# Performance work log

Hardware: AMD Instinct MI355X
Metric: run time of the kernel (lower is better)

Reference implementation:

```python
import jax, jax.numpy as jnp
import numpy as np

EPS = 1e-5

def conv1x1(x, W, b):
    # x: (B,C,H,W), W: (O,C), b: (O,)
    return jnp.einsum('bchw,oc->bohw', x, W) + b[None, :, None, None]

def setup_inputs() -> dict:
    key = jax.random.key(0)
    ks = jax.random.split(key, 16)
    B, C_in, C1, D, K, H, Wd = 8, 512, 256, 128, 32, 96, 96
    s = lambda k, shape, fan: jax.random.normal(k, shape, jnp.float32) * (1.0 / np.sqrt(fan))
    return {
        'X': jax.random.normal(ks[0], (B, C_in, H, Wd), jnp.float32),
        'W_theta': s(ks[1], (C1, C_in), C_in), 'b_theta': jnp.zeros((C1,), jnp.float32),
        'W_phi': s(ks[2], (C1, C_in), C_in), 'b_phi': jnp.zeros((C1,), jnp.float32),
        'W_g': s(ks[3], (C1, C_in), C_in), 'b_g': jnp.zeros((C1,), jnp.float32),
        'W2': s(ks[4], (C_in, C1), C1), 'b2': jnp.zeros((C_in,), jnp.float32),
        'W3': s(ks[5], (D, C_in), C_in), 'b3': jnp.zeros((D,), jnp.float32),
        'codewords': jax.random.normal(ks[6], (K, D), jnp.float32),
        'scale': -jax.random.uniform(ks[7], (K,), jnp.float32),  # Deep-TEN init: U(-1,0)
        'W_fc': s(ks[8], (C_in, D), D), 'b_fc': jnp.zeros((C_in,), jnp.float32),
    }

def reference(X, W_theta, b_theta, W_phi, b_phi, W_g, b_g, W2, b2, W3, b3,
              codewords, scale, W_fc, b_fc):
    B, C_in, H, Wd = X.shape
    C1 = W_theta.shape[0]
    D, K = W3.shape[0], codewords.shape[0]
    N = H * Wd
    # --- non-local (channel-attention) block ---
    theta = conv1x1(X, W_theta, b_theta).reshape(B, C1, N)          # (B,C1,N)
    phi = conv1x1(X, W_phi, b_phi).reshape(B, C1, N)                # (B,C1,N)
    g = conv1x1(X, W_g, b_g).reshape(B, C1, N)                      # (B,C1,N)
    f = jax.nn.softmax(jnp.einsum('bcn,bdn->bcd', theta, phi), axis=-1)  # (B,C1,C1)
    y = jnp.einsum('bcd,bdn->bcn', f, g).reshape(B, C1, H, Wd)
    z = conv1x1(y, W2, b2) + X                                      # (B,C_in,H,W)
    # --- Deep-TEN encoding ---
    z_ = conv1x1(z, W3, b3)                                         # (B,D,H,W)
    x = z_.reshape(B, D, N).transpose(0, 2, 1)                      # (B,N,D)
    # squared L2 distances to codewords without (B,N,K,D) residuals
    dist = (jnp.sum(x * x, -1, keepdims=True)
            - 2.0 * jnp.einsum('bnd,kd->bnk', x, codewords)
            + jnp.sum(codewords * codewords, -1))                   # (B,N,K)
    A = jax.nn.softmax(scale * dist, axis=-1)                       # (B,N,K)
    # E_k = sum_i A_ik (x_i - c_k)
    E = jnp.einsum('bnk,bnd->bkd', A, x) - A.sum(1)[..., None] * codewords  # (B,K,D)
    # --- training-mode batch norm over K channels (no affine) ---
    mean = E.mean(axis=(0, 2), keepdims=True)
    var = E.var(axis=(0, 2), keepdims=True)
    e = jax.nn.relu((E - mean) * jax.lax.rsqrt(var + EPS))
    Es = e.sum(axis=1)                                              # (B,D)
    gamma = jax.nn.sigmoid(Es @ W_fc.T + b_fc)                      # (B,C_in)
    return z * gamma[:, :, None, None]
```

## Files before the change

### kernel.cpp

```cpp
#include <hip/hip_runtime.h>


typedef unsigned short u16;

#define Bb 8
#define Cc 512
#define C1 256
#define Dd 128
#define Kk 32
#define Nn 9216

typedef __attribute__((ext_vector_type(8))) short short8v;
typedef __attribute__((ext_vector_type(4))) short short4v;
typedef __attribute__((ext_vector_type(4))) float f32x4;

__device__ __forceinline__ float b2f(u16 u) {
  union { unsigned int i; float f; } v; v.i = ((unsigned int)u) << 16; return v.f;
}
__device__ __forceinline__ u16 f2b(float f) {
  union { float f; unsigned int i; } v; v.f = f;
  unsigned int x = v.i;
  return (u16)((x + 0x7fffu + ((x >> 16) & 1u)) >> 16);
}

__device__ __forceinline__ float4 load4(const float* p) { return *(const float4*)p; }
__device__ __forceinline__ float4 load4(const u16* p) {
  ushort4 q = *(const ushort4*)p;
  return make_float4(b2f(q.x), b2f(q.y), b2f(q.z), b2f(q.w));
}
__device__ __forceinline__ void store4(float* p, float a, float b, float c, float d) {
  *(float4*)p = make_float4(a, b, c, d);
}

__device__ __forceinline__ float waveSum(float v) {
  #pragma unroll
  for (int o = 32; o > 0; o >>= 1) v += __shfl_xor(v, o);
  return v;
}
__device__ __forceinline__ float waveMax(float v) {
  #pragma unroll
  for (int o = 32; o > 0; o >>= 1) v = fmaxf(v, __shfl_xor(v, o));
  return v;
}
__device__ __forceinline__ float blockSum256(float v) {
  __shared__ float sm[4];
  v = waveSum(v);
  if ((threadIdx.x & 63) == 0) sm[threadIdx.x >> 6] = v;
  __syncthreads();
  float r = sm[0] + sm[1] + sm[2] + sm[3];
  __syncthreads();
  return r;
}
__device__ __forceinline__ float blockMax256(float v) {
  __shared__ float sm[4];
  v = waveMax(v);
  if ((threadIdx.x & 63) == 0) sm[threadIdx.x >> 6] = v;
  __syncthreads();
  float r = fmaxf(fmaxf(sm[0], sm[1]), fmaxf(sm[2], sm[3]));
  __syncthreads();
  return r;
}

__device__ __forceinline__ f32x4 mfma_bf16_16x16x32(short8v a, short8v b, f32x4 c) {
  asm("v_mfma_f32_16x16x32_bf16 %0, %1, %2, %0" : "+v"(c) : "v"(a), "v"(b));
  return c;
}

__device__ __forceinline__ int fsw(int r) { return (r ^ (r >> 2) ^ (r >> 4)) & 3; }

__device__ __forceinline__ void cvt2(float x0, float x1, unsigned int& h, unsigned int& l) {
  asm("v_cvt_pk_bf16_f32 %0, %1, %2" : "=v"(h) : "v"(x0), "v"(x1));
  union { unsigned int u; float f; } fa, fb;
  fa.u = h << 16; fb.u = h & 0xffff0000u;
  float r0 = x0 - fa.f, r1 = x1 - fb.f;
  asm("v_cvt_pk_bf16_f32 %0, %1, %2" : "=v"(l) : "v"(r0), "v"(r1));
}

__device__ __forceinline__ void storeC4(float* p, float4 v) { *(float4*)p = v; }
__device__ __forceinline__ void storeC4(u16* p, float4 v) {
  ushort4 q; q.x = f2b(v.x); q.y = f2b(v.y); q.z = f2b(v.z); q.w = f2b(v.w);
  *(ushort4*)p = q;
}

template<typename TO, int OMODE, bool ADDI>
__global__ __launch_bounds__(256, 3) void gemm_mfma(
    const float* __restrict__ A, const float* __restrict__ B, TO* __restrict__ C,
    int N, int K,
    long long sA, long long sB, long long sC,
    const float* __restrict__ biasRow, long long sBias,
    int gnx, int gny)
{
  __shared__ __align__(16) u16 Asm_[2][128][40];
  __shared__ __align__(16) u16 Bsm_[2][128][40];

  int id = blockIdx.x;
  {
    const int nwg = gridDim.x;
    if ((nwg & 7) == 0) id = (id & 7) * (nwg >> 3) + (id >> 3);
  }
  const int per = gnx * gny;
  const int b = id / per;
  const int rem = id - b * per;
  const int by = rem % gny;
  const int bx = rem / gny;
  A += b * sA; B += b * sB; C += b * sC;
  const int m0 = by * 128, n0 = bx * 128;

  const int t = threadIdx.x;
  const int w = t >> 6, lane = t & 63;
  const int wr = w >> 1, wc = w & 1;
  const int lr = lane & 15, lq = lane >> 4;

  const int sar = t >> 1, sak = (t & 1) * 16;
  const int kg2 = t >> 4, ng = t & 15;

  float ra[16];
  float rb[16];

  auto loadA = [&](int k0) {
    const float* p = A + (long long)(m0 + sar) * K + (k0 + sak);
    #pragma unroll
    for (int i = 0; i < 4; ++i) {
      float4 v = *(const float4*)(p + i * 4);
      ra[i*4+0] = v.x; ra[i*4+1] = v.y; ra[i*4+2] = v.z; ra[i*4+3] = v.w;
    }
  };
  auto loadB = [&](int k0) {
    const float* p = B + (long long)(k0 + kg2 * 2) * N + (n0 + ng * 8);
    #pragma unroll
    for (int i = 0; i < 2; ++i) {
      float4 v0 = *(const float4*)(p + (long long)i * N);
      float4 v1 = *(const float4*)(p + (long long)i * N + 4);
      rb[i*8+0]=v0.x; rb[i*8+1]=v0.y; rb[i*8+2]=v0.z; rb[i*8+3]=v0.w;
      rb[i*8+4]=v1.x; rb[i*8+5]=v1.y; rb[i*8+6]=v1.z; rb[i*8+7]=v1.w;
    }
  };

  auto stage = [&]() {
    {
      const int f = fsw(sar);
      #pragma unroll
      for (int h = 0; h < 2; ++h) {
        const int col = ((((sak >> 3) + h) ^ f) << 3);
        union { unsigned int u[4]; short8v v; } H, L;
        #pragma unroll
        for (int p = 0; p < 4; ++p) cvt2(ra[h*8+2*p], ra[h*8+2*p+1], H.u[p], L.u[p]);
        *(short8v*)&Asm_[0][sar][col] = H.v;
        *(short8v*)&Asm_[1][sar][col] = L.v;
      }
    }
    {
      const int blk = kg2 >> 2, sub = 2 * (kg2 & 3);
      #pragma unroll
      for (int j = 0; j < 8; ++j) {
        const int n = ng * 8 + j;
        const int col = ((blk ^ fsw(n)) << 3) + sub;
        unsigned int H, L;
        cvt2(rb[j], rb[8 + j], H, L);
        *(unsigned int*)&Bsm_[0][n][col] = H;
        *(unsigned int*)&Bsm_[1][n][col] = L;
      }
    }
  };

  f32x4 acc[4][4];
  #pragma unroll
  for (int im = 0; im < 4; ++im)
    #pragma unroll
    for (int in = 0; in < 4; ++in)
      acc[im][in] = f32x4{0.f, 0.f, 0.f, 0.f};

  loadA(0); loadB(0);
  for (int k0 = 0; k0 < K; k0 += 32) {
    stage();
    if (k0 + 32 < K) { loadA(k0 + 32); loadB(k0 + 32); }
    __syncthreads();
    short8v af[2][4];
    #pragma unroll
    for (int im = 0; im < 4; ++im) {
      const int r = wr * 64 + im * 16 + lr;
      const int col = ((lq ^ fsw(r)) << 3);
      af[0][im] = *(const short8v*)&Asm_[0][r][col];
      af[1][im] = *(const short8v*)&Asm_[1][r][col];
    }
    #pragma unroll
    for (int in = 0; in < 4; ++in) {
      const int rB = wc * 64 + in * 16 + lr;
      const int colB = ((lq ^ fsw(rB)) << 3);
      short8v bh = *(const short8v*)&Bsm_[0][rB][colB];
      short8v bl = *(const short8v*)&Bsm_[1][rB][colB];
      #pragma unroll
      for (int im = 0; im < 4; ++im) {
        acc[im][in] = mfma_bf16_16x16x32(af[0][im], bh, acc[im][in]);
        acc[im][in] = mfma_bf16_16x16x32(af[0][im], bl, acc[im][in]);
        acc[im][in] = mfma_bf16_16x16x32(af[1][im], bh, acc[im][in]);
      }
    }
    __syncthreads();
  }
  asm volatile("s_nop 7\n\ts_nop 7\n\ts_nop 7");

  if constexpr (OMODE == 1) {
    const float* bb = biasRow + (long long)b * sBias;
    #pragma unroll
    for (int im = 0; im < 4; ++im) {
      #pragma unroll
      for (int in = 0; in < 4; ++in) {
        const f32x4 a = acc[im][in];
        const int gc = n0 + wc * 64 + in * 16 + lr;
        const int d0b = wr * 64 + im * 16 + lq * 4;
        float4 v = make_float4(a[0] + bb[d0b + 0], a[1] + bb[d0b + 1],
                               a[2] + bb[d0b + 2], a[3] + bb[d0b + 3]);
        storeC4(&C[(long long)gc * Dd + d0b], v);
      }
    }
  } else {
    #pragma unroll
    for (int im = 0; im < 4; ++im) {
      #pragma unroll
      for (int in = 0; in < 4; ++in) {
        const f32x4 a = acc[im][in];
        const int gc = n0 + wc * 64 + in * 16 + lr;
        #pragma unroll
        for (int p = 0; p < 4; ++p) {
          const int gr = m0 + wr * 64 + im * 16 + lq * 4 + p;
          float v = a[p];
          if (biasRow) v += biasRow[b * sBias + gr];
          if (ADDI && gr == gc) v += 1.f;
          C[(long long)gr * N + gc] = v;
        }
      }
    }
  }
}

__device__ __constant__ int PIa[10] = {0,0,0,0,1,1,1,2,2,3};
__device__ __constant__ int PJa[10] = {0,1,2,3,1,2,3,2,3,3};

__global__ __launch_bounds__(256, 3) void gxxt_kernel(
    const float* __restrict__ X, float* __restrict__ part,
    int numKS, int kChunk)
{
  __shared__ __align__(16) u16 Asm_[2][128][40];
  __shared__ __align__(16) u16 Bsm_[2][64][40];

  int id = blockIdx.x;
  {
    const int nwg = gridDim.x;
    if ((nwg & 7) == 0) id = (id & 7) * (nwg >> 3) + (id >> 3);
  }
  const int sub = id % 20;
  const int pair = sub >> 1, jh = sub & 1;
  const int rest = id / 20;
  const int ks = rest % numKS;
  const int b = rest / numKS;
  const int i0 = PIa[pair] * 128, j0 = PJa[pair] * 128;
  const bool same = (i0 == j0);
  const float* Xb = X + (long long)b * Cc * Nn;
  const int kBeg = ks * kChunk, kEnd = kBeg + kChunk;

  const int t = threadIdx.x;
  const int w = t >> 6, lane = t & 63;
  const int wr = w >> 1, wc = w & 1;
  const int lr = lane & 15, lq = lane >> 4;
  const int sar = t >> 1, sak = (t & 1) * 16;
  const int sbr = t >> 2, sbk = (t & 3) * 8;

  float ra[16], rb[8];

  auto loadA = [&](int k0) {
    const float* p = Xb + (long long)(i0 + sar) * Nn + (k0 + sak);
    #pragma unroll
    for (int i = 0; i < 4; ++i) {
      float4 v = *(const float4*)(p + i * 4);
      ra[i*4+0] = v.x; ra[i*4+1] = v.y; ra[i*4+2] = v.z; ra[i*4+3] = v.w;
    }
  };
  auto loadB = [&](int k0) {
    const float* p = Xb + (long long)(j0 + jh * 64 + sbr) * Nn + (k0 + sbk);
    float4 v0 = *(const float4*)(p);
    float4 v1 = *(const float4*)(p + 4);
    rb[0]=v0.x; rb[1]=v0.y; rb[2]=v0.z; rb[3]=v0.w;
    rb[4]=v1.x; rb[5]=v1.y; rb[6]=v1.z; rb[7]=v1.w;
  };
  auto stageA = [&]() {
    const int f = fsw(sar);
    #pragma unroll
    for (int h = 0; h < 2; ++h) {
      const int col = ((((sak >> 3) + h) ^ f) << 3);
      union { unsigned int u[4]; short8v v; } Hv, Lv;
      #pragma unroll
      for (int p = 0; p < 4; ++p) cvt2(ra[h*8+2*p], ra[h*8+2*p+1], Hv.u[p], Lv.u[p]);
      *(short8v*)&Asm_[0][sar][col] = Hv.v;
      *(short8v*)&Asm_[1][sar][col] = Lv.v;
    }
  };
  auto stageB = [&]() {
    const int col = (((sbk >> 3) ^ fsw(sbr)) << 3);
    union { unsigned int u[4]; short8v v; } Hv, Lv;
    #pragma unroll
    for (int p = 0; p < 4; ++p) cvt2(rb[2*p], rb[2*p+1], Hv.u[p], Lv.u[p]);
    *(short8v*)&Bsm_[0][sbr][col] = Hv.v;
    *(short8v*)&Bsm_[1][sbr][col] = Lv.v;
  };

  f32x4 acc[4][2];
  #pragma unroll
  for (int im = 0; im < 4; ++im)
    #pragma unroll
    for (int in = 0; in < 2; ++in)
      acc[im][in] = f32x4{0.f, 0.f, 0.f, 0.f};

  loadA(kBeg);
  if (!same) loadB(kBeg);
  for (int k0 = kBeg; k0 < kEnd; k0 += 32) {
    stageA();
    if (!same) stageB();
    if (k0 + 32 < kEnd) { loadA(k0 + 32); if (!same) loadB(k0 + 32); }
    __syncthreads();
    short8v af[2][4];
    #pragma unroll
    for (int im = 0; im < 4; ++im) {
      const int r = wr * 64 + im * 16 + lr;
      const int col = ((lq ^ fsw(r)) << 3);
      af[0][im] = *(const short8v*)&Asm_[0][r][col];
      af[1][im] = *(const short8v*)&Asm_[1][r][col];
    }
    #pragma unroll
    for (int in = 0; in < 2; ++in) {
      const int rloc = wc * 32 + in * 16 + lr;
      short8v bh, bl;
      if (same) {
        const int r = jh * 64 + rloc;
        const int colB = ((lq ^ fsw(r)) << 3);
        bh = *(const short8v*)&Asm_[0][r][colB];
        bl = *(const short8v*)&Asm_[1][r][colB];
      } else {
        const int colB = ((lq ^ fsw(rloc)) << 3);
        bh = *(const short8v*)&Bsm_[0][rloc][colB];
        bl = *(const short8v*)&Bsm_[1][rloc][colB];
      }
      #pragma unroll
      for (int im = 0; im < 4; ++im) {
        acc[im][in] = mfma_bf16_16x16x32(af[0][im], bh, acc[im][in]);
        acc[im][in] = mfma_bf16_16x16x32(af[0][im], bl, acc[im][in]);
        acc[im][in] = mfma_bf16_16x16x32(af[1][im], bh, acc[im][in]);
      }
    }
    __syncthreads();
  }
  asm volatile("s_nop 7\n\ts_nop 7\n\ts_nop 7");

  float* Cp = part + ((long long)(ks * Bb + b) * 10 + pair) * 16384 + jh * 64;
  #pragma unroll
  for (int im = 0; im < 4; ++im) {
    #pragma unroll
    for (int in = 0; in < 2; ++in) {
      const f32x4 a = acc[im][in];
      const int gc = wc * 32 + in * 16 + lr;
      #pragma unroll
      for (int p = 0; p < 4; ++p) {
        const int gr = wr * 64 + im * 16 + lq * 4 + p;
        Cp[gr * 128 + gc] = a[p];
      }
    }
  }
}

__global__ __launch_bounds__(256) void gred_kernel(const float* __restrict__ part,
    float* __restrict__ G, int numKS) {
  __shared__ float sm[64][129];
  const int pair = blockIdx.x % 10, b = blockIdx.x / 10;
  const int i0 = PIa[pair] * 128, j0 = PJa[pair] * 128;
  float* Gb = G + (long long)b * Cc * Cc;
  const long long ksStr = (long long)Bb * 10 * 16384;
  const float* p0 = part + ((long long)b * 10 + pair) * 16384;
  const int t = threadIdx.x;
  for (int half = 0; half < 2; ++half) {
    const int r0 = half * 64;
    __syncthreads();
    for (int rep = 0; rep < 32; ++rep) {
      int idx = r0 * 128 + rep * 256 + t;
      float s = 0.f;
      for (int ks = 0; ks < numKS; ++ks) s += p0[(long long)ks * ksStr + idx];
      int r = (idx >> 7) - r0, c = idx & 127;
      sm[r][c] = s;
      Gb[(long long)(i0 + r0 + r) * Cc + (j0 + c)] = s;
    }
    if (i0 != j0) {
      __syncthreads();
      for (int rep = 0; rep < 32; ++rep) {
        int o = rep * 256 + t;
        int rr = o >> 6, cc = o & 63;
        Gb[(long long)(j0 + rr) * Cc + (i0 + r0 + cc)] = sm[cc][rr];
      }
    }
  }
}

template<bool TRANSB>
__global__ __launch_bounds__(256) void gemm64(
    const float* __restrict__ A, const float* __restrict__ B, float* __restrict__ C,
    int M, int N, int K,
    long long sA, long long sB, long long sC,
    const float* __restrict__ biasRow, long long sBias)
{
  const int bz = blockIdx.z;
  A += (long long)bz * sA;
  B += (long long)bz * sB;
  C += (long long)bz * sC;
  const int m0 = blockIdx.y * 64, n0 = blockIdx.x * 64;
  __shared__ __align__(16) float As[16][64];
  __shared__ __align__(16) float Bs[16][64];
  const int t = threadIdx.x;
  const int lr = t >> 2, lk = (t & 3) << 2;
  const int tm = (t >> 4) << 2, tn = (t & 15) << 2;
  float acc[4][4] = {};
  for (int k0 = 0; k0 < K; k0 += 16) {
    {
      float4 a = load4(A + (long long)(m0 + lr) * K + (k0 + lk));
      As[lk + 0][lr] = a.x; As[lk + 1][lr] = a.y; As[lk + 2][lr] = a.z; As[lk + 3][lr] = a.w;
    }
    if (TRANSB) {
      float4 b = load4(B + (long long)(n0 + lr) * K + (k0 + lk));
      Bs[lk + 0][lr] = b.x; Bs[lk + 1][lr] = b.y; Bs[lk + 2][lr] = b.z; Bs[lk + 3][lr] = b.w;
    } else {
      const int kr = t >> 4, nc = (t & 15) << 2;
      float4 b = load4(B + (long long)(k0 + kr) * N + (n0 + nc));
      *(float4*)&Bs[kr][nc] = b;
    }
    __syncthreads();
    #pragma unroll
    for (int kk = 0; kk < 16; ++kk) {
      const float4 av = *(const float4*)&As[kk][tm];
      const float4 bv = *(const float4*)&Bs[kk][tn];
      acc[0][0] = fmaf(av.x, bv.x, acc[0][0]);
      acc[0][1] = fmaf(av.x, bv.y, acc[0][1]);
      acc[0][2] = fmaf(av.x, bv.z, acc[0][2]);
      acc[0][3] = fmaf(av.x, bv.w, acc[0][3]);
      acc[1][0] = fmaf(av.y, bv.x, acc[1][0]);
      acc[1][1] = fmaf(av.y, bv.y, acc[1][1]);
      acc[1][2] = fmaf(av.y, bv.z, acc[1][2]);
      acc[1][3] = fmaf(av.y, bv.w, acc[1][3]);
      acc[2][0] = fmaf(av.z, bv.x, acc[2][0]);
      acc[2][1] = fmaf(av.z, bv.y, acc[2][1]);
      acc[2][2] = fmaf(av.z, bv.z, acc[2][2]);
      acc[2][3] = fmaf(av.z, bv.w, acc[2][3]);
      acc[3][0] = fmaf(av.w, bv.x, acc[3][0]);
      acc[3][1] = fmaf(av.w, bv.y, acc[3][1]);
      acc[3][2] = fmaf(av.w, bv.z, acc[3][2]);
      acc[3][3] = fmaf(av.w, bv.w, acc[3][3]);
    }
    __syncthreads();
  }
  #pragma unroll
  for (int i = 0; i < 4; ++i) {
    const int m = m0 + tm + i;
    float bias = biasRow ? biasRow[bz * sBias + m] : 0.f;
    store4(C + (long long)m * N + (n0 + tn),
           acc[i][0] + bias, acc[i][1] + bias, acc[i][2] + bias, acc[i][3] + bias);
  }
}

__global__ __launch_bounds__(256) void rowsum_kernel(const float* __restrict__ X,
                                                     float* __restrict__ s, int N) {
  long long row = blockIdx.x;
  const float* p = X + row * N;
  float acc = 0.f;
  for (int i = threadIdx.x * 4; i < N; i += 1024) {
    float4 v = *(const float4*)(p + i);
    acc += (v.x + v.y) + (v.z + v.w);
  }
  acc = blockSum256(acc);
  if (threadIdx.x == 0) s[row] = acc;
}

__global__ __launch_bounds__(256) void gemv2_kernel(const float* __restrict__ Wth,
    const float* __restrict__ Wph, const float* __restrict__ s,
    float* __restrict__ u, float* __restrict__ v) {
  int b = blockIdx.x & 7, sel = blockIdx.x >> 3;
  const float* W = sel ? Wph : Wth;
  float* out = sel ? v : u;
  __shared__ float ssm[Cc];
  for (int i = threadIdx.x; i < Cc; i += 256) ssm[i] = s[b * Cc + i];
  __syncthreads();
  int i = threadIdx.x;
  const float* wr = W + i * Cc;
  float acc = 0.f;
  for (int k = 0; k < Cc; ++k) acc = fmaf(wr[k], ssm[k], acc);
  out[b * C1 + i] = acc;
}

__global__ __launch_bounds__(256) void softmax_kernel(float* __restrict__ L,
    const float* __restrict__ bth, const float* __restrict__ bph,
    const float* __restrict__ u, const float* __restrict__ v,
    const float* __restrict__ bg, float* __restrict__ w) {
  __shared__ float bgs[C1];
  int row = blockIdx.x;
  int b = row >> 8, i = row & 255;
  int j = threadIdx.x;
  bgs[j] = bg[j];
  float bt = bth[i], bp = bph[j];
  long long idx = (long long)row * C1 + j;
  float val = L[idx] + bt * v[b * C1 + j] + u[b * C1 + i] * bp + (float)Nn * bt * bp;
  float mx = blockMax256(val);
  float p = expf(val - mx);
  float sm = blockSum256(p);
  float f = p / sm;
  L[idx] = f;
  float ws = blockSum256(f * bgs[j]);
  if (j == 0) w[row] = ws;
}

__global__ __launch_bounds__(256) void q_kernel(const float* __restrict__ W2,
                                                const float* __restrict__ b2v,
                                                const float* __restrict__ w,
                                                float* __restrict__ q) {
  int gi = blockIdx.x * 256 + threadIdx.x;
  int b = gi >> 9, c = gi & 511;
  __shared__ float wsm[C1];
  wsm[threadIdx.x] = w[b * C1 + threadIdx.x];
  __syncthreads();
  const float* wr = W2 + c * C1;
  float acc = b2v[c];
  for (int i = 0; i < C1; ++i) acc = fmaf(wr[i], wsm[i], acc);
  q[gi] = acc;
}

__global__ __launch_bounds__(256) void zqbias_kernel(const float* __restrict__ W3,
    const float* __restrict__ b3, const float* __restrict__ q, float* __restrict__ zqb) {
  int gi = blockIdx.x * 256 + threadIdx.x;
  int b = gi >> 7, d = gi & 127;
  const float* wr = W3 + d * Cc;
  const float* qr = q + b * Cc;
  float acc = b3[d];
  for (int c = 0; c < Cc; ++c) acc = fmaf(wr[c], qr[c], acc);
  zqb[gi] = acc;
}

template<typename ZT>
__global__ __launch_bounds__(256) void enc_kernel(
    const ZT* __restrict__ zq,
    const float* __restrict__ cw,
    const float* __restrict__ sc,
    float* __restrict__ Eraw8,
    float* __restrict__ Asum8)
{
  __shared__ float csm[Kk][Dd + 1];
  __shared__ float cc[Kk], ssm[Kk];
  __shared__ float sA[Kk][256 + 1];
  __shared__ float zs[16][Dd + 4];
  const int tid = threadIdx.x;
  const int b = blockIdx.y;
  const int slot = blockIdx.x & 7;
  const int n0 = blockIdx.x * 256;

  #pragma unroll
  for (int r = 0; r < 16; ++r) {
    int idx = r * 256 + tid;
    csm[idx >> 7][idx & 127] = cw[idx];
  }
  if (tid < Kk) ssm[tid] = sc[tid];
  __syncthreads();
  if (tid < Kk) {
    float a = 0.f;
    for (int d = 0; d < Dd; ++d) { float cv = csm[tid][d]; a = fmaf(cv, cv, a); }
    cc[tid] = a;
  }
  __syncthreads();

  const ZT* zrow = zq + ((long long)b * Nn + n0 + tid) * Dd;
  float dots[Kk];
  #pragma unroll
  for (int k = 0; k < Kk; ++k) dots[k] = 0.f;
  float xx = 0.f;
  for (int d = 0; d < Dd; d += 4) {
    float4 xv = load4(zrow + d);
    xx = fmaf(xv.x, xv.x, xx); xx = fmaf(xv.y, xv.y, xx);
    xx = fmaf(xv.z, xv.z, xx); xx = fmaf(xv.w, xv.w, xx);
    #pragma unroll
    for (int k = 0; k < Kk; ++k) {
      float dk = dots[k];
      dk = fmaf(csm[k][d + 0], xv.x, dk);
      dk = fmaf(csm[k][d + 1], xv.y, dk);
      dk = fmaf(csm[k][d + 2], xv.z, dk);
      dk = fmaf(csm[k][d + 3], xv.w, dk);
      dots[k] = dk;
    }
  }
  float mx = -1e30f;
  #pragma unroll
  for (int k = 0; k < Kk; ++k) {
    float l = ssm[k] * (xx - 2.f * dots[k] + cc[k]);
    dots[k] = l;
    mx = fmaxf(mx, l);
  }
  float sum = 0.f;
  #pragma unroll
  for (int k = 0; k < Kk; ++k) { float p = expf(dots[k] - mx); dots[k] = p; sum += p; }
  float inv = 1.f / sum;
  #pragma unroll
  for (int k = 0; k < Kk; ++k) sA[k][tid] = dots[k] * inv;
  __syncthreads();
  if (tid < Kk) {
    float s = 0.f;
    for (int p = 0; p < 256; ++p) s += sA[tid][p];
    atomicAdd(&Asum8[((long long)slot * Bb + b) * Kk + tid], s);
  }

  float acc[16];
  #pragma unroll
  for (int j = 0; j < 16; ++j) acc[j] = 0.f;
  const int k = tid & 31, d0 = (tid >> 5) * 16;
  const int spx = tid >> 4, sd = (tid & 15) * 8;
  for (int it = 0; it < 16; ++it) {
    __syncthreads();
    {
      const ZT* src = zq + ((long long)b * Nn + n0 + it * 16 + spx) * Dd + sd;
      float4 a4 = load4(src);
      float4 b4 = load4(src + 4);
      *(float4*)&zs[spx][sd] = a4;
      *(float4*)&zs[spx][sd + 4] = b4;
    }
    __syncthreads();
    #pragma unroll
    for (int p = 0; p < 16; ++p) {
      float a = sA[k][it * 16 + p];
      #pragma unroll
      for (int j = 0; j < 16; ++j) acc[j] = fmaf(a, zs[p][d0 + j], acc[j]);
    }
  }
  float* Ep = Eraw8 + (((long long)slot * Bb + b) * Kk + k) * Dd + d0;
  #pragma unroll
  for (int j = 0; j < 16; ++j) atomicAdd(Ep + j, acc[j]);
}

__global__ __launch_bounds__(256) void bn_kernel(const float* __restrict__ Eraw8,
    const float* __restrict__ Asum8, const float* __restrict__ cw, float* __restrict__ Es) {
  __shared__ float sas[8];
  int k = blockIdx.x, tid = threadIdx.x;
  if (tid < 8) {
    float a = 0.f;
    for (int sl = 0; sl < 8; ++sl) a += Asum8[((long long)sl * Bb + tid) * Kk + k];
    sas[tid] = a;
  }
  __syncthreads();
  float vals[4], s = 0.f, s2 = 0.f;
  #pragma unroll
  for (int r = 0; r < 4; ++r) {
    int i = r * 256 + tid;
    int b = i >> 7, d = i & 127;
    float e = 0.f;
    for (int sl = 0; sl < 8; ++sl)
      e += Eraw8[(((long long)sl * Bb + b) * Kk + k) * Dd + d];
    e -= sas[b] * cw[k * Dd + d];
    vals[r] = e; s += e; s2 = fmaf(e, e, s2);
  }
  s = blockSum256(s);
  s2 = blockSum256(s2);
  float mean = s * (1.f / 1024.f);
  float var = fmaxf(s2 * (1.f / 1024.f) - mean * mean, 0.f);
  float rs = rsqrtf(var + 1e-5f);
  #pragma unroll
  for (int r = 0; r < 4; ++r) {
    int i = r * 256 + tid;
    int b = i >> 7, d = i & 127;
    float e = (vals[r] - mean) * rs;
    if (e > 0.f) atomicAdd(&Es[b * Dd + d], e);
  }
}

__global__ __launch_bounds__(256) void gamma_kernel(const float* __restrict__ Es,
    const float* __restrict__ Wfc, const float* __restrict__ bfc,
    float* __restrict__ gam, float* __restrict__ q) {
  int gi = blockIdx.x * 256 + threadIdx.x;
  int b = gi >> 9, c = gi & 511;
  __shared__ float esm[Dd];
  if (threadIdx.x < Dd) esm[threadIdx.x] = Es[b * Dd + threadIdx.x];
  __syncthreads();
  const float* wr = Wfc + c * Dd;
  float acc = bfc[c];
  for (int d = 0; d < Dd; ++d) acc = fmaf(wr[d], esm[d], acc);
  float g = 1.f / (1.f + expf(-acc));
  gam[gi] = g;
  q[gi] *= g;
}

__global__ __launch_bounds__(256) void scaleP_kernel(float* __restrict__ P,
    const float* __restrict__ gam) {
  long long f = ((long long)blockIdx.x * 256 + threadIdx.x) * 4;
  int b = (int)(f >> 18), c = (int)((f >> 9) & 511);
  float g = gam[b * Cc + c];
  float4 v = *(const float4*)(P + f);
  store4(P + f, v.x * g, v.y * g, v.z * g, v.w * g);
}

extern "C" void kernel_launch(void* const* d_in, const int* in_sizes, int n_in,
                              void* d_out, int out_size, void* d_ws, size_t ws_size,
                              hipStream_t stream) {
  const float* X   = (const float*)d_in[0];
  const float* Wth = (const float*)d_in[1];
  const float* bth = (const float*)d_in[2];
  const float* Wph = (const float*)d_in[3];
  const float* bph = (const float*)d_in[4];
  const float* Wg  = (const float*)d_in[5];
  const float* bg  = (const float*)d_in[6];
  const float* W2  = (const float*)d_in[7];
  const float* b2v = (const float*)d_in[8];
  const float* W3  = (const float*)d_in[9];
  const float* b3v = (const float*)d_in[10];
  const float* CW  = (const float*)d_in[11];
  const float* SC  = (const float*)d_in[12];
  const float* Wfc = (const float*)d_in[13];
  const float* bfc = (const float*)d_in[14];
  float* out = (float*)d_out;
  float* wsf = (float*)d_ws;

  const long long szL   = (long long)Bb * C1 * C1;
  const long long szRA  = (long long)Bb * Cc * Cc;
  const long long szRB  = (long long)Bb * C1 * Cc;
  long long off = 0;
  float* s_   = wsf + off; off += Bb * Cc;
  float* u_   = wsf + off; off += Bb * C1;
  float* v_   = wsf + off; off += Bb * C1;
  float* w_   = wsf + off; off += Bb * C1;
  float* q_   = wsf + off; off += Bb * Cc;
  float* Eraw_= wsf + off; off += (long long)Bb * Kk * Dd;
  float* Es_  = wsf + off; off += Bb * Dd;
  float* Asum_= wsf + off; off += Bb * Kk;
  float* gam_ = wsf + off; off += Bb * Cc;
  float* L_   = wsf + off; off += szL;
  float* regA = wsf + off; off += szRA;
  float* regB = wsf + off; off += szRB;
  const long long baseFloats = off;
  float* tail = wsf + off;
  const long long ZQ_F  = (long long)Bb * Dd * Nn;
  const long long tailFloats = (long long)(ws_size / 4) - baseFloats;
  const bool big = tailFloats >= ZQ_F;
  const int numKS = big ? 6 : 2;
  float* part = tail;
  float* zqf  = tail;
  u16*   zqh  = (u16*)tail;
  float* R_   = L_;
  float* zqb_ = u_;
  float* E8_  = regB;
  float* A8_  = regB + 262144;
  (void)Eraw_; (void)Asum_;

  const long long strX = (long long)Cc * Nn;
  const long long sG = (long long)Cc * Cc;
  const long long sU = (long long)C1 * Cc;
  const long long sL = (long long)C1 * C1;
  const long long sR = (long long)Dd * Cc;

  rowsum_kernel<<<Bb * Cc, 256, 0, stream>>>(X, s_, Nn);
  gxxt_kernel<<<dim3(20 * numKS * Bb), 256, 0, stream>>>(X, part, numKS, Nn / numKS);
  gred_kernel<<<dim3(10 * Bb), 256, 0, stream>>>(part, regA, numKS);
  gemm_mfma<float, 0, false><<<dim3(64), 256, 0, stream>>>(
      Wth, regA, regB, Cc, Cc, 0, sG, sU, nullptr, 0, 4, 2);
  gemv2_kernel<<<16, 256, 0, stream>>>(Wth, Wph, s_, u_, v_);
  gemm64<true><<<dim3(4, 4, Bb), 256, 0, stream>>>(
      regB, Wph, L_, C1, C1, Cc, sU, 0, sL, nullptr, 0);
  softmax_kernel<<<Bb * C1, 256, 0, stream>>>(L_, bth, bph, u_, v_, bg, w_);
  gemm_mfma<float, 0, false><<<dim3(64), 256, 0, stream>>>(
      L_, Wg, regB, Cc, C1, sL, 0, sU, nullptr, 0, 4, 2);
  q_kernel<<<16, 256, 0, stream>>>(W2, b2v, w_, q_);
  gemm_mfma<float, 0, true><<<dim3(128), 256, 0, stream>>>(
      W2, regB, regA, Cc, C1, 0, sU, sG, nullptr, 0, 4, 4);
  hipMemsetAsync(regB, 0, (size_t)(262144 + 2048) * 4, stream);
  hipMemsetAsync(Es_, 0, (size_t)(Bb * Dd) * 4, stream);
  gemm_mfma<float, 0, false><<<dim3(32), 256, 0, stream>>>(
      W3, regA, R_, Cc, Cc, 0, sG, sR, nullptr, 0, 4, 1);
  zqbias_kernel<<<4, 256, 0, stream>>>(W3, b3v, q_, zqb_);
  if (big) {
    gemm_mfma<float, 1, false><<<dim3(576), 256, 0, stream>>>(
        R_, X, zqf, Nn, Cc, sR, strX, (long long)Dd * Nn, zqb_, Dd, 72, 1);
    enc_kernel<float><<<dim3(36, Bb), 256, 0, stream>>>(zqf, CW, SC, E8_, A8_);
  } else {
    gemm_mfma<u16, 1, false><<<dim3(576), 256, 0, stream>>>(
        R_, X, zqh, Nn, Cc, sR, strX, (long long)Dd * Nn, zqb_, Dd, 72, 1);
    enc_kernel<u16><<<dim3(36, Bb), 256, 0, stream>>>(zqh, CW, SC, E8_, A8_);
  }
  bn_kernel<<<Kk, 256, 0, stream>>>(E8_, A8_, CW, Es_);
  gamma_kernel<<<16, 256, 0, stream>>>(Es_, Wfc, bfc, gam_, q_);
  scaleP_kernel<<<2048, 256, 0, stream>>>(regA, gam_);
  gemm_mfma<float, 0, false><<<dim3(2304), 256, 0, stream>>>(
      regA, X, out, Nn, Cc, sG, strX, strX, q_, Cc, 72, 4);
  (void)in_sizes; (void)n_in; (void)out_size;
}
```

Baseline: 957.8 us.

## Fuse rowsum into Gram kernel, fold gamma scaling into final GEMM, pad B LDS

Result: no change. 947.5 us (-1.1%).

```diff
diff --git a/kernel.cpp b/kernel.cpp
--- a/kernel.cpp
+++ b/kernel.cpp
@@ -10,6 +10,8 @@
 #define Kk 32
 #define Nn 9216
 
+#define BIDX(n, c) (((n) * 40) + (((n) >> 3) * 8) + (c))
+
 typedef __attribute__((ext_vector_type(8))) short short8v;
 typedef __attribute__((ext_vector_type(4))) short short4v;
 typedef __attribute__((ext_vector_type(4))) float f32x4;
@@ -88,10 +90,11 @@
     int N, int K,
     long long sA, long long sB, long long sC,
     const float* __restrict__ biasRow, long long sBias,
+    const float* __restrict__ scaleA,
     int gnx, int gny)
 {
   __shared__ __align__(16) u16 Asm_[2][128][40];
-  __shared__ __align__(16) u16 Bsm_[2][128][40];
+  __shared__ __align__(16) u16 Bsm_[2][5248];
 
   int id = blockIdx.x;
   {
@@ -114,6 +117,8 @@
   const int sar = t >> 1, sak = (t & 1) * 16;
   const int kg2 = t >> 4, ng = t & 15;
 
+  const float gA = scaleA ? scaleA[b * sBias + m0 + sar] : 1.f;
+
   float ra[16];
   float rb[16];
 
@@ -144,7 +149,8 @@
         const int col = ((((sak >> 3) + h) ^ f) << 3);
         union { unsigned int u[4]; short8v v; } H, L;
         #pragma unroll
-        for (int p = 0; p < 4; ++p) cvt2(ra[h*8+2*p], ra[h*8+2*p+1], H.u[p], L.u[p]);
+        for (int p = 0; p < 4; ++p)
+          cvt2(ra[h*8+2*p] * gA, ra[h*8+2*p+1] * gA, H.u[p], L.u[p]);
         *(short8v*)&Asm_[0][sar][col] = H.v;
         *(short8v*)&Asm_[1][sar][col] = L.v;
       }
@@ -157,8 +163,8 @@
         const int col = ((blk ^ fsw(n)) << 3) + sub;
         unsigned int H, L;
         cvt2(rb[j], rb[8 + j], H, L);
-        *(unsigned int*)&Bsm_[0][n][col] = H;
-        *(unsigned int*)&Bsm_[1][n][col] = L;
+        *(unsigned int*)&Bsm_[0][BIDX(n, col)] = H;
+        *(unsigned int*)&Bsm_[1][BIDX(n, col)] = L;
       }
     }
   };
@@ -187,8 +193,8 @@
     for (int in = 0; in < 4; ++in) {
       const int rB = wc * 64 + in * 16 + lr;
       const int colB = ((lq ^ fsw(rB)) << 3);
-      short8v bh = *(const short8v*)&Bsm_[0][rB][colB];
-      short8v bl = *(const short8v*)&Bsm_[1][rB][colB];
+      short8v bh = *(const short8v*)&Bsm_[0][BIDX(rB, colB)];
+      short8v bl = *(const short8v*)&Bsm_[1][BIDX(rB, colB)];
       #pragma unroll
       for (int im = 0; im < 4; ++im) {
         acc[im][in] = mfma_bf16_16x16x32(af[0][im], bh, acc[im][in]);
@@ -239,10 +245,10 @@
 
 __global__ __launch_bounds__(256, 3) void gxxt_kernel(
     const float* __restrict__ X, float* __restrict__ part,
-    int numKS, int kChunk)
+    int numKS, int kChunk, float* __restrict__ sOut)
 {
   __shared__ __align__(16) u16 Asm_[2][128][40];
-  __shared__ __align__(16) u16 Bsm_[2][64][40];
+  __shared__ __align__(16) u16 Bsm_[2][2624];
 
   int id = blockIdx.x;
   {
@@ -256,6 +262,7 @@
   const int b = rest / numKS;
   const int i0 = PIa[pair] * 128, j0 = PJa[pair] * 128;
   const bool same = (i0 == j0);
+  const bool doSum = same && (jh == 0);
   const float* Xb = X + (long long)b * Cc * Nn;
   const int kBeg = ks * kChunk, kEnd = kBeg + kChunk;
 
@@ -267,6 +274,7 @@
   const int sbr = t >> 2, sbk = (t & 3) * 8;
 
   float ra[16], rb[8];
+  float rs = 0.f;
 
   auto loadA = [&](int k0) {
     const float* p = Xb + (long long)(i0 + sar) * Nn + (k0 + sak);
@@ -300,8 +308,8 @@
     union { unsigned int u[4]; short8v v; } Hv, Lv;
     #pragma unroll
     for (int p = 0; p < 4; ++p) cvt2(rb[2*p], rb[2*p+1], Hv.u[p], Lv.u[p]);
-    *(short8v*)&Bsm_[0][sbr][col] = Hv.v;
-    *(short8v*)&Bsm_[1][sbr][col] = Lv.v;
+    *(short8v*)&Bsm_[0][BIDX(sbr, col)] = Hv.v;
+    *(short8v*)&Bsm_[1][BIDX(sbr, col)] = Lv.v;
   };
 
   f32x4 acc[4][2];
@@ -314,6 +322,10 @@
   loadA(kBeg);
   if (!same) loadB(kBeg);
   for (int k0 = kBeg; k0 < kEnd; k0 += 32) {
+    if (doSum) {
+      #pragma unroll
+      for (int j = 0; j < 16; ++j) rs += ra[j];
+    }
     stageA();
     if (!same) stageB();
     if (k0 + 32 < kEnd) { loadA(k0 + 32); if (!same) loadB(k0 + 32); }
@@ -337,8 +349,8 @@
         bl = *(const short8v*)&Asm_[1][r][colB];
       } else {
         const int colB = ((lq ^ fsw(rloc)) << 3);
-        bh = *(const short8v*)&Bsm_[0][rloc][colB];
-        bl = *(const short8v*)&Bsm_[1][rloc][colB];
+        bh = *(const short8v*)&Bsm_[0][BIDX(rloc, colB)];
+        bl = *(const short8v*)&Bsm_[1][BIDX(rloc, colB)];
       }
       #pragma unroll
       for (int im = 0; im < 4; ++im) {
@@ -350,6 +362,8 @@
     __syncthreads();
   }
   asm volatile("s_nop 7\n\ts_nop 7\n\ts_nop 7");
+
+  if (doSum) atomicAdd(&sOut[b * Cc + i0 + sar], rs);
 
   float* Cp = part + ((long long)(ks * Bb + b) * 10 + pair) * 16384 + jh * 64;
   #pragma unroll
@@ -462,19 +476,6 @@
   }
 }
 
-__global__ __launch_bounds__(256) void rowsum_kernel(const float* __restrict__ X,
-                                                     float* __restrict__ s, int N) {
-  long long row = blockIdx.x;
-  const float* p = X + row * N;
-  float acc = 0.f;
-  for (int i = threadIdx.x * 4; i < N; i += 1024) {
-    float4 v = *(const float4*)(p + i);
-    acc += (v.x + v.y) + (v.z + v.w);
-  }
-  acc = blockSum256(acc);
-  if (threadIdx.x == 0) s[row] = acc;
-}
-
 __global__ __launch_bounds__(256) void gemv2_kernel(const float* __restrict__ Wth,
     const float* __restrict__ Wph, const float* __restrict__ s,
     float* __restrict__ u, float* __restrict__ v) {
@@ -684,15 +685,6 @@
   float g = 1.f / (1.f + expf(-acc));
   gam[gi] = g;
   q[gi] *= g;
-}
-
-__global__ __launch_bounds__(256) void scaleP_kernel(float* __restrict__ P,
-    const float* __restrict__ gam) {
-  long long f = ((long long)blockIdx.x * 256 + threadIdx.x) * 4;
-  int b = (int)(f >> 18), c = (int)((f >> 9) & 511);
-  float g = gam[b * Cc + c];
-  float4 v = *(const float4*)(P + f);
-  store4(P + f, v.x * g, v.y * g, v.z * g, v.w * g);
 }
 
 extern "C" void kernel_launch(void* const* d_in, const int* in_sizes, int n_in,
@@ -726,7 +718,7 @@
   float* w_   = wsf + off; off += Bb * C1;
   float* q_   = wsf + off; off += Bb * Cc;
   float* Eraw_= wsf + off; off += (long long)Bb * Kk * Dd;
-  float* Es_  = wsf + off; off += Bb * Dd;
+  float* EsL_ = wsf + off; off += Bb * Dd;
   float* Asum_= wsf + off; off += Bb * Kk;
   float* gam_ = wsf + off; off += Bb * Cc;
   float* L_   = wsf + off; off += szL;
@@ -737,7 +729,7 @@
   const long long ZQ_F  = (long long)Bb * Dd * Nn;
   const long long tailFloats = (long long)(ws_size / 4) - baseFloats;
   const bool big = tailFloats >= ZQ_F;
-  const int numKS = big ? 6 : 2;
+  const int numKS = big ? 4 : 2;
   float* part = tail;
   float* zqf  = tail;
   u16*   zqh  = (u16*)tail;
@@ -745,7 +737,8 @@
   float* zqb_ = u_;
   float* E8_  = regB;
   float* A8_  = regB + 262144;
-  (void)Eraw_; (void)Asum_;
+  float* Es_  = regB + 264192;
+  (void)Eraw_; (void)Asum_; (void)EsL_;
 
   const long long strX = (long long)Cc * Nn;
   const long long sG = (long long)Cc * Cc;
@@ -753,38 +746,36 @@
   const long long sL = (long long)C1 * C1;
   const long long sR = (long long)Dd * Cc;
 
-  rowsum_kernel<<<Bb * Cc, 256, 0, stream>>>(X, s_, Nn);
-  gxxt_kernel<<<dim3(20 * numKS * Bb), 256, 0, stream>>>(X, part, numKS, Nn / numKS);
+  hipMemsetAsync(s_, 0, (size_t)(Bb * Cc) * 4, stream);
+  gxxt_kernel<<<dim3(20 * numKS * Bb), 256, 0, stream>>>(X, part, numKS, Nn / numKS, s_);
   gred_kernel<<<dim3(10 * Bb), 256, 0, stream>>>(part, regA, numKS);
   gemm_mfma<float, 0, false><<<dim3(64), 256, 0, stream>>>(
-      Wth, regA, regB, Cc, Cc, 0, sG, sU, nullptr, 0, 4, 2);
+      Wth, regA, regB, Cc, Cc, 0, sG, sU, nullptr, 0, nullptr, 4, 2);
   gemv2_kernel<<<16, 256, 0, stream>>>(Wth, Wph, s_, u_, v_);
   gemm64<true><<<dim3(4, 4, Bb), 256, 0, stream>>>(
       regB, Wph, L_, C1, C1, Cc, sU, 0, sL, nullptr, 0);
   softmax_kernel<<<Bb * C1, 256, 0, stream>>>(L_, bth, bph, u_, v_, bg, w_);
   gemm_mfma<float, 0, false><<<dim3(64), 256, 0, stream>>>(
-      L_, Wg, regB, Cc, C1, sL, 0, sU, nullptr, 0, 4, 2);
+      L_, Wg, regB, Cc, C1, sL, 0, sU, nullptr, 0, nullptr, 4, 2);
   q_kernel<<<16, 256, 0, stream>>>(W2, b2v, w_, q_);
   gemm_mfma<float, 0, true><<<dim3(128), 256, 0, stream>>>(
-      W2, regB, regA, Cc, C1, 0, sU, sG, nullptr, 0, 4, 4);
-  hipMemsetAsync(regB, 0, (size_t)(262144 + 2048) * 4, stream);
-  hipMemsetAsync(Es_, 0, (size_t)(Bb * Dd) * 4, stream);
+      W2, regB, regA, Cc, C1, 0, sU, sG, nullptr, 0, nullptr, 4, 4);
+  hipMemsetAsync(regB, 0, (size_t)(262144 + 2048 + 1024) * 4, stream);
   gemm_mfma<float, 0, false><<<dim3(32), 256, 0, stream>>>(
-      W3, regA, R_, Cc, Cc, 0, sG, sR, nullptr, 0, 4, 1);
+      W3, regA, R_, Cc, Cc, 0, sG, sR, nullptr, 0, nullptr, 4, 1);
   zqbias_kernel<<<4, 256, 0, stream>>>(W3, b3v, q_, zqb_);
   if (big) {
     gemm_mfma<float, 1, false><<<dim3(576), 256, 0, stream>>>(
-        R_, X, zqf, Nn, Cc, sR, strX, (long long)Dd * Nn, zqb_, Dd, 72, 1);
+        R_, X, zqf, Nn, Cc, sR, strX, (long long)Dd * Nn, zqb_, Dd, nullptr, 72, 1);
     enc_kernel<float><<<dim3(36, Bb), 256, 0, stream>>>(zqf, CW, SC, E8_, A8_);
   } else {
     gemm_mfma<u16, 1, false><<<dim3(576), 256, 0, stream>>>(
-        R_, X, zqh, Nn, Cc, sR, strX, (long long)Dd * Nn, zqb_, Dd, 72, 1);
+        R_, X, zqh, Nn, Cc, sR, strX, (long long)Dd * Nn, zqb_, Dd, nullptr, 72, 1);
     enc_kernel<u16><<<dim3(36, Bb), 256, 0, stream>>>(zqh, CW, SC, E8_, A8_);
   }
   bn_kernel<<<Kk, 256, 0, stream>>>(E8_, A8_, CW, Es_);
   gamma_kernel<<<16, 256, 0, stream>>>(Es_, Wfc, bfc, gam_, q_);
-  scaleP_kernel<<<2048, 256, 0, stream>>>(regA, gam_);
   gemm_mfma<float, 0, false><<<dim3(2304), 256, 0, stream>>>(
-      regA, X, out, Nn, Cc, sG, strX, strX, q_, Cc, 72, 4);
+      regA, X, out, Nn, Cc, sG, strX, strX, q_, Cc, gam_, 72, 4);
   (void)in_sizes; (void)n_in; (void)out_size;
 }
```

## Fuse X row sums into Gram kernel and merge memsets

Applied to the files above, without the earlier changes.

New measurement: 895.9 us. 6.5% less time.

```diff
diff --git a/kernel.cpp b/kernel.cpp
--- a/kernel.cpp
+++ b/kernel.cpp
@@ -239,7 +239,7 @@
 
 __global__ __launch_bounds__(256, 3) void gxxt_kernel(
     const float* __restrict__ X, float* __restrict__ part,
-    int numKS, int kChunk)
+    int numKS, int kChunk, float* __restrict__ sP)
 {
   __shared__ __align__(16) u16 Asm_[2][128][40];
   __shared__ __align__(16) u16 Bsm_[2][64][40];
@@ -256,6 +256,7 @@
   const int b = rest / numKS;
   const int i0 = PIa[pair] * 128, j0 = PJa[pair] * 128;
   const bool same = (i0 == j0);
+  const bool doSum = same && (jh == 0);
   const float* Xb = X + (long long)b * Cc * Nn;
   const int kBeg = ks * kChunk, kEnd = kBeg + kChunk;
 
@@ -267,6 +268,7 @@
   const int sbr = t >> 2, sbk = (t & 3) * 8;
 
   float ra[16], rb[8];
+  float rs = 0.f;
 
   auto loadA = [&](int k0) {
     const float* p = Xb + (long long)(i0 + sar) * Nn + (k0 + sak);
@@ -314,6 +316,10 @@
   loadA(kBeg);
   if (!same) loadB(kBeg);
   for (int k0 = kBeg; k0 < kEnd; k0 += 32) {
+    if (doSum) {
+      #pragma unroll
+      for (int j = 0; j < 16; ++j) rs += ra[j];
+    }
     stageA();
     if (!same) stageB();
     if (k0 + 32 < kEnd) { loadA(k0 + 32); if (!same) loadB(k0 + 32); }
@@ -350,6 +356,8 @@
     __syncthreads();
   }
   asm volatile("s_nop 7\n\ts_nop 7\n\ts_nop 7");
+
+  if (doSum) sP[((long long)ks * Bb + b) * Cc + i0 + sar] = rs;
 
   float* Cp = part + ((long long)(ks * Bb + b) * 10 + pair) * 16384 + jh * 64;
   #pragma unroll
@@ -462,27 +470,18 @@
   }
 }
 
-__global__ __launch_bounds__(256) void rowsum_kernel(const float* __restrict__ X,
-                                                     float* __restrict__ s, int N) {
-  long long row = blockIdx.x;
-  const float* p = X + row * N;
-  float acc = 0.f;
-  for (int i = threadIdx.x * 4; i < N; i += 1024) {
-    float4 v = *(const float4*)(p + i);
-    acc += (v.x + v.y) + (v.z + v.w);
-  }
-  acc = blockSum256(acc);
-  if (threadIdx.x == 0) s[row] = acc;
-}
-
 __global__ __launch_bounds__(256) void gemv2_kernel(const float* __restrict__ Wth,
-    const float* __restrict__ Wph, const float* __restrict__ s,
+    const float* __restrict__ Wph, const float* __restrict__ sP, int numKS,
     float* __restrict__ u, float* __restrict__ v) {
   int b = blockIdx.x & 7, sel = blockIdx.x >> 3;
   const float* W = sel ? Wph : Wth;
   float* out = sel ? v : u;
   __shared__ float ssm[Cc];
-  for (int i = threadIdx.x; i < Cc; i += 256) ssm[i] = s[b * Cc + i];
+  for (int i = threadIdx.x; i < Cc; i += 256) {
+    float s = 0.f;
+    for (int ks = 0; ks < numKS; ++ks) s += sP[((long long)ks * Bb + b) * Cc + i];
+    ssm[i] = s;
+  }
   __syncthreads();
   int i = threadIdx.x;
   const float* wr = W + i * Cc;
@@ -725,8 +724,8 @@
   float* v_   = wsf + off; off += Bb * C1;
   float* w_   = wsf + off; off += Bb * C1;
   float* q_   = wsf + off; off += Bb * Cc;
-  float* Eraw_= wsf + off; off += (long long)Bb * Kk * Dd;
-  float* Es_  = wsf + off; off += Bb * Dd;
+  float* sP_  = wsf + off; off += (long long)Bb * Kk * Dd;
+  float* EsL_ = wsf + off; off += Bb * Dd;
   float* Asum_= wsf + off; off += Bb * Kk;
   float* gam_ = wsf + off; off += Bb * Cc;
   float* L_   = wsf + off; off += szL;
@@ -737,7 +736,7 @@
   const long long ZQ_F  = (long long)Bb * Dd * Nn;
   const long long tailFloats = (long long)(ws_size / 4) - baseFloats;
   const bool big = tailFloats >= ZQ_F;
-  const int numKS = big ? 6 : 2;
+  const int numKS = big ? 4 : 2;
   float* part = tail;
   float* zqf  = tail;
   u16*   zqh  = (u16*)tail;
@@ -745,7 +744,8 @@
   float* zqb_ = u_;
   float* E8_  = regB;
   float* A8_  = regB + 262144;
-  (void)Eraw_; (void)Asum_;
+  float* Es_  = regB + 264192;
+  (void)s_; (void)Asum_; (void)EsL_;
 
   const long long strX = (long long)Cc * Nn;
   const long long sG = (long long)Cc * Cc;
@@ -753,12 +753,11 @@
   const long long sL = (long long)C1 * C1;
   const long long sR = (long long)Dd * Cc;
 
-  rowsum_kernel<<<Bb * Cc, 256, 0, stream>>>(X, s_, Nn);
-  gxxt_kernel<<<dim3(20 * numKS * Bb), 256, 0, stream>>>(X, part, numKS, Nn / numKS);
+  gxxt_kernel<<<dim3(20 * numKS * Bb), 256, 0, stream>>>(X, part, numKS, Nn / numKS, sP_);
   gred_kernel<<<dim3(10 * Bb), 256, 0, stream>>>(part, regA, numKS);
   gemm_mfma<float, 0, false><<<dim3(64), 256, 0, stream>>>(
       Wth, regA, regB, Cc, Cc, 0, sG, sU, nullptr, 0, 4, 2);
-  gemv2_kernel<<<16, 256, 0, stream>>>(Wth, Wph, s_, u_, v_);
+  gemv2_kernel<<<16, 256, 0, stream>>>(Wth, Wph, sP_, numKS, u_, v_);
   gemm64<true><<<dim3(4, 4, Bb), 256, 0, stream>>>(
       regB, Wph, L_, C1, C1, Cc, sU, 0, sL, nullptr, 0);
   softmax_kernel<<<Bb * C1, 256, 0, stream>>>(L_, bth, bph, u_, v_, bg, w_);
@@ -767,8 +766,7 @@
   q_kernel<<<16, 256, 0, stream>>>(W2, b2v, w_, q_);
   gemm_mfma<float, 0, true><<<dim3(128), 256, 0, stream>>>(
       W2, regB, regA, Cc, C1, 0, sU, sG, nullptr, 0, 4, 4);
-  hipMemsetAsync(regB, 0, (size_t)(262144 + 2048) * 4, stream);
-  hipMemsetAsync(Es_, 0, (size_t)(Bb * Dd) * 4, stream);
+  hipMemsetAsync(regB, 0, (size_t)(262144 + 2048 + 1024) * 4, stream);
   gemm_mfma<float, 0, false><<<dim3(32), 256, 0, stream>>>(
       W3, regA, R_, Cc, Cc, 0, sG, sR, nullptr, 0, 4, 1);
   zqbias_kernel<<<4, 256, 0, stream>>>(W3, b3v, q_, zqb_);
```
